# Kernel tuning notes

Hardware: AMD Instinct MI355X
Metric: run time of the kernel (lower is better)

## Reference

```python
import jax, jax.numpy as jnp
import numpy as np


def _dilate(x, ker):
    """Grayscale (max-plus) dilation, TF tf.nn.dilation2d semantics, SAME pad, stride 1.

    x:   [B,H,W,C] or [B,H,W,C,F]
    ker: [kh,kw,C,F]
    out: [B,H,W,C,F] = max_{dy,dx} x_pad[b, h+dy, w+dx, c(,f)] + ker[dy,dx,c,f]
    """
    kh, kw = ker.shape[0], ker.shape[1]
    pt, pl = (kh - 1) // 2, (kw - 1) // 2
    pb, pr = kh - 1 - pt, kw - 1 - pl
    if x.ndim == 4:
        x = x[..., None]  # broadcast over filter axis
    B, H, W = x.shape[0], x.shape[1], x.shape[2]
    xp = jnp.pad(x, ((0, 0), (pt, pb), (pl, pr), (0, 0), (0, 0)),
                 constant_values=-jnp.inf)
    out = None
    for dy in range(kh):
        for dx in range(kw):
            v = xp[:, dy:dy + H, dx:dx + W] + ker[dy, dx]  # [B,H,W,C,F]
            out = v if out is None else jnp.maximum(out, v)
    return out


def _erode(x, ker):
    # TF identity: erosion2d(v, f) = -dilation2d(-v, spatially-flipped f)
    return -_dilate(-x, ker[::-1, ::-1])


def _opening_p4(x, kernel):
    # x: [B,4,H,W,C], kernel: [kh,kw,3,C,F]
    kero = jnp.stack([jnp.rot90(kernel[:, :, 2], 3, axes=(0, 1)),
                      kernel[:, :, 1],
                      jnp.rot90(kernel[:, :, 0], 1, axes=(0, 1))], axis=2)
    y = jnp.concatenate([x[:, -1:], x, x[:, :1]], axis=1)  # wrap group axis -> [B,6,H,W,C]
    ero = []
    for j in range(4):
        kr = jnp.rot90(kero, j, axes=(0, 1))  # [kh,kw,3,C,F]
        d = jnp.stack([_erode(y[:, j + k], kr[:, :, k]) for k in range(3)], axis=-1)
        ero.append(jnp.min(d, axis=-1))  # min over SE depth -> [B,H,W,C,F]
    ero = jnp.stack(ero, axis=1)  # [B,4,H,W,C,F]
    ep = jnp.concatenate([ero[:, -1:], ero, ero[:, :1]], axis=1)  # [B,6,H,W,C,F]
    outs = []
    for j in range(4):
        kr = jnp.rot90(kernel, j, axes=(0, 1))
        d = jnp.stack([_dilate(ep[:, j + k], kr[:, :, k]) for k in range(3)], axis=-1)
        outs.append(jnp.max(d, axis=-1))  # max over SE depth -> [B,H,W,C,F]
    open_res = jnp.stack(outs, axis=1)  # [B,4,H,W,C,F]
    return jnp.sum(open_res, axis=-2)   # sum over input channels -> [B,4,H,W,F]


def setup_inputs() -> dict:
    key = jax.random.key(0)
    k1, k2 = jax.random.split(key)
    x = jax.random.normal(k1, (4, 4, 64, 64, 8), dtype=jnp.float32)
    kernel = jax.random.normal(k2, (3, 3, 3, 8, 16), dtype=jnp.float32) * 0.1
    return {"x": x, "kernel": kernel}


def reference(x, kernel):
    return _opening_p4(x, kernel)
```

## Files before the change

### kernel.cpp

```cpp
#include <hip/hip_runtime.h>


#define HH 64
#define WW 64
#define NEG_INF (-__builtin_inff())
#define POS_INF (__builtin_inff())

#define ROT_G(G, A, B, I, J) do { switch (G) { \
    case 0:  I = (A);     J = (B);     break; \
    case 1:  I = (B);     J = 2 - (A); break; \
    case 2:  I = 2 - (A); J = 2 - (B); break; \
    default: I = 2 - (B); J = (A);     break; } } while (0)

typedef _Float16 hv4 __attribute__((ext_vector_type(4)));

__device__ __forceinline__ hv4 f4_to_hv4(float4 v) {
    hv4 r;
    r.x = (_Float16)v.x; r.y = (_Float16)v.y;
    r.z = (_Float16)v.z; r.w = (_Float16)v.w;
    return r;
}

__device__ __forceinline__ hv4 bcast16(float v) {
    _Float16 p = (_Float16)v;
    return (hv4){p, p, p, p};
}

__global__ __launch_bounds__(256) void erode_t(const float* __restrict__ x,
                                               const float* __restrict__ ker,
                                               hv4* __restrict__ ero) {
    __shared__ __align__(16) float xs[9 * 8 * 68];

    const int tid = threadIdx.x;
    const int h = blockIdx.x & 63;
    const int g = (blockIdx.x >> 6) & 3;
    const int b = blockIdx.x >> 8;

    const float4* x4 = (const float4*)x;
    const float4* ker4 = (const float4*)ker;

    for (int t = tid; t < 1188; t += 256) {
        int q01 = t & 1;
        int u = t >> 1;
        int wp = u % 66;
        int v = u / 66;
        int r = v % 3;
        int p = v / 3;
        int g2 = (g + p + 3) & 3;
        int h2 = h - 1 + r;
        int w2 = wp - 1;
        float4 vv;
        if ((unsigned)h2 < HH && (unsigned)w2 < WW)
            vv = x4[(((b * 4 + g2) * HH + h2) * WW + w2) * 2 + q01];
        else
            vv = make_float4(POS_INF, POS_INF, POS_INF, POS_INF);
        int rowb = (p * 3 + r) * 8 + q01 * 4;
        xs[(rowb + 0) * 68 + wp] = vv.x;
        xs[(rowb + 1) * 68 + wp] = vv.y;
        xs[(rowb + 2) * 68 + wp] = vv.z;
        xs[(rowb + 3) * 68 + wp] = vv.w;
    }
    __syncthreads();

    const int q = tid & 3;
    const int c = (tid >> 2) & 7;
    const int slot = tid >> 5;
    const float4* xs4 = (const float4*)xs;

    const _Float16 pinf16 = (_Float16)POS_INF;
    hv4 acc[8];
#pragma unroll
    for (int i = 0; i < 8; ++i)
        acc[i] = (hv4){pinf16, pinf16, pinf16, pinf16};

#pragma unroll
    for (int k2 = 0; k2 < 3; ++k2) {
        hv4 ke9[9];
#pragma unroll
        for (int t9 = 0; t9 < 9; ++t9) {
            int dy = t9 / 3, dx = t9 % 3;
            int a0 = 2 - dy, b0 = 2 - dx;
            int i, jj;
            ROT_G(g, a0, b0, i, jj);
            int ka, kb, kc;
            if (k2 == 0)      { ka = 2 - jj; kb = i;      kc = 2; }
            else if (k2 == 1) { ka = i;      kb = jj;     kc = 1; }
            else              { ka = jj;     kb = 2 - i;  kc = 0; }
            ke9[t9] = f4_to_hv4(ker4[((ka * 3 + kb) * 3 + kc) * 32 + c * 4 + q]);
        }
#pragma unroll
        for (int dy = 0; dy < 3; ++dy) {
            const int base4 = ((k2 * 3 + dy) * 8 + c) * 17 + slot * 2;
            float4 xa = xs4[base4];
            float4 xb = xs4[base4 + 1];
            float4 xc = xs4[base4 + 2];
            float xw[12] = {xa.x, xa.y, xa.z, xa.w,
                            xb.x, xb.y, xb.z, xb.w,
                            xc.x, xc.y, xc.z, xc.w};
            hv4 xv[12];
#pragma unroll
            for (int i = 0; i < 12; ++i)
                xv[i] = bcast16(xw[i]);
#pragma unroll
            for (int dx = 0; dx < 3; ++dx) {
                hv4 kv = ke9[dy * 3 + dx];
#pragma unroll
                for (int i = 0; i < 8; ++i)
                    acc[i] = __builtin_elementwise_min(acc[i], xv[i + dx] - kv);
            }
        }
    }

    const int row = (b * 4 + g) * HH + h;
    const size_t obase = ((size_t)row * 66 + slot * 8 + 1) * 32 + c * 4 + q;
#pragma unroll
    for (int i = 0; i < 8; ++i)
        ero[obase + (size_t)i * 32] = acc[i];

    const hv4 ninf = {(_Float16)NEG_INF, (_Float16)NEG_INF,
                      (_Float16)NEG_INF, (_Float16)NEG_INF};
    if (tid < 32)
        ero[(size_t)row * 66 * 32 + tid] = ninf;
    else if (tid < 64)
        ero[((size_t)row * 66 + 65) * 32 + (tid - 32)] = ninf;
}

__global__ __launch_bounds__(256) void dilate_t(const hv4* __restrict__ ero,
                                                const float* __restrict__ ker,
                                                float* __restrict__ out) {
    const int tid = threadIdx.x;
    const int q = tid & 3;
    const int c = (tid >> 2) & 7;
    const int slot = tid >> 5;
    const int ws = blockIdx.x & 7;
    const int hs = (blockIdx.x >> 3) & 7;
    const int j = (blockIdx.x >> 6) & 3;
    const int b = blockIdx.x >> 8;
    const int w = ws * 8 + slot;

    const float4* ker4 = (const float4*)ker;

    const hv4 ninf = {(_Float16)NEG_INF, (_Float16)NEG_INF,
                      (_Float16)NEG_INF, (_Float16)NEG_INF};
    hv4 acc[8];
#pragma unroll
    for (int r = 0; r < 8; ++r)
        acc[r] = ninf;

#pragma unroll
    for (int k = 0; k < 3; ++k) {
        const int gsrc = (j + k + 3) & 3;
        hv4 kd9[9];
#pragma unroll
        for (int t9 = 0; t9 < 9; ++t9) {
            int dy = t9 / 3, dx = t9 % 3;
            int i, jj;
            ROT_G(j, dy, dx, i, jj);
            kd9[t9] = f4_to_hv4(ker4[((i * 3 + jj) * 3 + k) * 32 + c * 4 + q]);
        }
        const size_t pb = ((size_t)(b * 4 + gsrc) * HH * 66 + w) * 32 + c * 4 + q;
#pragma unroll
        for (int ei = 0; ei < 10; ++ei) {
            const int er = hs * 8 - 1 + ei;
            if ((unsigned)er >= HH) continue;
            const size_t rb = pb + (size_t)er * 66 * 32;
            hv4 e0 = ero[rb];
            hv4 e1 = ero[rb + 32];
            hv4 e2 = ero[rb + 64];
#pragma unroll
            for (int dy = 0; dy < 3; ++dy) {
                const int rr = ei - dy;
                if ((unsigned)rr >= 8) continue;
                acc[rr] = __builtin_elementwise_max(acc[rr], e0 + kd9[dy * 3 + 0]);
                acc[rr] = __builtin_elementwise_max(acc[rr], e1 + kd9[dy * 3 + 1]);
                acc[rr] = __builtin_elementwise_max(acc[rr], e2 + kd9[dy * 3 + 2]);
            }
        }
    }

    float4* out4 = (float4*)out;
    const int bjbase = (b * 4 + j) * HH + hs * 8;
#pragma unroll
    for (int r = 0; r < 8; ++r) {
        float4 s = make_float4((float)acc[r].x, (float)acc[r].y,
                               (float)acc[r].z, (float)acc[r].w);
#pragma unroll
        for (int off = 4; off <= 16; off <<= 1) {
            s.x += __shfl_xor(s.x, off, 64);
            s.y += __shfl_xor(s.y, off, 64);
            s.z += __shfl_xor(s.z, off, 64);
            s.w += __shfl_xor(s.w, off, 64);
        }
        if (c == 0)
            out4[((size_t)(bjbase + r) * WW + w) * 4 + q] = s;
    }
}

__global__ __launch_bounds__(256, 3) void opening_fused_fb(
    const float* __restrict__ x, const float* __restrict__ ker, float* __restrict__ out)
{
    __shared__ __align__(16) float xs[8 * 4 * 144];
    __shared__ float4 es4[4 * 4 * 100];
    __shared__ float4 ke4[27 * 4 * 4];
    __shared__ float4 kd4[9 * 4 * 4];

    const int tid = threadIdx.x;
    const int tileX = blockIdx.x & 7;
    const int tileY = (blockIdx.x >> 3) & 7;
    const int j = (blockIdx.x >> 6) & 3;
    const int b = blockIdx.x >> 8;
    const float4* ker4 = (const float4*)ker;
    const float4* x4 = (const float4*)x;

    for (int t = tid; t < 1152; t += 256) {
        int q01 = t & 1;
        int cell = t >> 1;
        int g = cell / 144;
        int rem = cell - g * 144;
        int r = rem / 12;
        int s = rem - r * 12;
        int h = tileY * 8 - 2 + r;
        int w = tileX * 8 - 2 + s;
        float4 v;
        if ((unsigned)h < HH && (unsigned)w < WW)
            v = x4[(((b * 4 + g) * HH + h) * WW + w) * 2 + q01];
        else
            v = make_float4(POS_INF, POS_INF, POS_INF, POS_INF);
        int c0 = q01 * 4;
        xs[((c0 + 0) * 4 + g) * 144 + rem] = v.x;
        xs[((c0 + 1) * 4 + g) * 144 + rem] = v.y;
        xs[((c0 + 2) * 4 + g) * 144 + rem] = v.z;
        xs[((c0 + 3) * 4 + g) * 144 + rem] = v.w;
    }
    __syncthreads();

    const int q_o = tid & 3;
    const int ox = (tid >> 2) & 7;
    const int oy = tid >> 5;

    float4 acc[8];
#pragma unroll
    for (int c = 0; c < 8; ++c)
        acc[c] = make_float4(NEG_INF, NEG_INF, NEG_INF, NEG_INF);

    for (int k = 0; k < 3; ++k) {
        const int gsrc = (j + k + 3) & 3;
#pragma unroll
        for (int cg = 0; cg < 2; ++cg) {
            for (int t = tid; t < 576; t += 256) {
                if (t < 432) {
                    int q = t & 3;
                    int c4 = (t >> 2) & 3;
                    int tap = t >> 4;
                    int k2 = tap % 3;
                    int dxdy = tap / 3;
                    int dx = dxdy % 3;
                    int dy = dxdy / 3;
                    int a0 = 2 - dy, b0 = 2 - dx;
                    int i, jj;
                    ROT_G(gsrc, a0, b0, i, jj);
                    int ka, kb, kc;
                    if (k2 == 0)      { ka = 2 - jj; kb = i;      kc = 2; }
                    else if (k2 == 1) { ka = i;      kb = jj;     kc = 1; }
                    else              { ka = jj;     kb = 2 - i;  kc = 0; }
                    int c = cg * 4 + c4;
                    ke4[t] = ker4[((ka * 3 + kb) * 3 + kc) * 32 + c * 4 + q];
                } else {
                    int u = t - 432;
                    int q = u & 3;
                    int c4 = (u >> 2) & 3;
                    int dydx = u >> 4;
                    int dx = dydx % 3;
                    int dy = dydx / 3;
                    int i, jj;
                    ROT_G(j, dy, dx, i, jj);
                    int c = cg * 4 + c4;
                    kd4[u] = ker4[((i * 3 + jj) * 3 + k) * 32 + c * 4 + q];
                }
            }
            __syncthreads();

            for (int it = 0; it < 2; ++it) {
                int id = tid + (it << 8);
                int c4 = id >> 7;
                int p = id & 127;
                if (p >= 100) continue;
                int ey = (p * 205) >> 11;
                int ex = p - ey * 10;
                int h_es = tileY * 8 - 1 + ey;
                int w_es = tileX * 8 - 1 + ex;
                float4 b0, b1, b2, b3;
                if ((unsigned)h_es < HH && (unsigned)w_es < WW) {
                    b0 = b1 = b2 = b3 = make_float4(POS_INF, POS_INF, POS_INF, POS_INF);
                    int c = cg * 4 + c4;
#pragma unroll
                    for (int k2 = 0; k2 < 3; ++k2) {
                        int g2 = (gsrc + k2 + 3) & 3;
                        int base = (c * 4 + g2) * 144 + ey * 12 + ex;
#pragma unroll
                        for (int dy = 0; dy < 3; ++dy)
#pragma unroll
                            for (int dx = 0; dx < 3; ++dx) {
                                float v = xs[base + dy * 12 + dx];
                                const float4* kk = &ke4[(((dy * 3 + dx) * 3 + k2) * 4 + c4) * 4];
                                float4 kv;
                                kv = kk[0];
                                b0.x = fminf(b0.x, v - kv.x); b0.y = fminf(b0.y, v - kv.y);
                                b0.z = fminf(b0.z, v - kv.z); b0.w = fminf(b0.w, v - kv.w);
                                kv = kk[1];
                                b1.x = fminf(b1.x, v - kv.x); b1.y = fminf(b1.y, v - kv.y);
                                b1.z = fminf(b1.z, v - kv.z); b1.w = fminf(b1.w, v - kv.w);
                                kv = kk[2];
                                b2.x = fminf(b2.x, v - kv.x); b2.y = fminf(b2.y, v - kv.y);
                                b2.z = fminf(b2.z, v - kv.z); b2.w = fminf(b2.w, v - kv.w);
                                kv = kk[3];
                                b3.x = fminf(b3.x, v - kv.x); b3.y = fminf(b3.y, v - kv.y);
                                b3.z = fminf(b3.z, v - kv.z); b3.w = fminf(b3.w, v - kv.w);
                            }
                    }
                } else {
                    b0 = b1 = b2 = b3 = make_float4(NEG_INF, NEG_INF, NEG_INF, NEG_INF);
                }
                int eb = (c4 * 4) * 100 + p;
                es4[eb] = b0; es4[eb + 100] = b1; es4[eb + 200] = b2; es4[eb + 300] = b3;
            }
            __syncthreads();

#pragma unroll
            for (int c4 = 0; c4 < 4; ++c4) {
                float4 a = acc[cg * 4 + c4];
#pragma unroll
                for (int dy = 0; dy < 3; ++dy)
#pragma unroll
                    for (int dx = 0; dx < 3; ++dx) {
                        int pos = (oy + dy) * 10 + (ox + dx);
                        float4 e = es4[(c4 * 4 + q_o) * 100 + pos];
                        float4 kv = kd4[(dy * 3 + dx) * 16 + c4 * 4 + q_o];
                        a.x = fmaxf(a.x, e.x + kv.x);
                        a.y = fmaxf(a.y, e.y + kv.y);
                        a.z = fmaxf(a.z, e.z + kv.z);
                        a.w = fmaxf(a.w, e.w + kv.w);
                    }
                acc[cg * 4 + c4] = a;
            }
            __syncthreads();
        }
    }

    float4 s = acc[0];
#pragma unroll
    for (int c = 1; c < 8; ++c) {
        s.x += acc[c].x; s.y += acc[c].y; s.z += acc[c].z; s.w += acc[c].w;
    }
    const int h = tileY * 8 + oy;
    const int w = tileX * 8 + ox;
    ((float4*)out)[(((b * 4 + j) * HH + h) * WW + w) * 4 + q_o] = s;
}

extern "C" void kernel_launch(void* const* d_in, const int* in_sizes, int n_in,
                              void* d_out, int out_size, void* d_ws, size_t ws_size,
                              hipStream_t stream) {
    const float* x = (const float*)d_in[0];
    const float* ker = (const float*)d_in[1];
    float* out = (float*)d_out;

    const size_t ero_f16_bytes = (size_t)16 * HH * 66 * 32 * 8;

    if (ws_size >= ero_f16_bytes) {
        hv4* ero = (hv4*)d_ws;
        erode_t<<<1024, 256, 0, stream>>>(x, ker, ero);
        dilate_t<<<1024, 256, 0, stream>>>(ero, ker, out);
    } else {
        opening_fused_fb<<<1024, 256, 0, stream>>>(x, ker, out);
    }
}
```

Baseline: 91.92 us.

## Compute all four output rotations per dilate block to reuse eroded rows

The dilate kernel now loops over each source group once and scatters its contribution into all three output rotations that depend on it, holding accumulators for all four rotations at four rows each. Each eroded row is loaded once per source group instead of being reloaded for every output rotation, which cuts global/L2 traffic. The price is more registers (16 accumulators plus 27 kernel vectors), a smaller grid of 512 blocks, and a larger relative halo with 4-row tiles.

```diff
diff --git a/kernel.cpp b/kernel.cpp
--- a/kernel.cpp
+++ b/kernel.cpp
@@ -125,75 +125,87 @@
         ero[((size_t)row * 66 + 65) * 32 + (tid - 32)] = ninf;
 }
 
-__global__ __launch_bounds__(256) void dilate_t(const hv4* __restrict__ ero,
-                                                const float* __restrict__ ker,
-                                                float* __restrict__ out) {
+__global__ __launch_bounds__(256) void dilate_j4(const hv4* __restrict__ ero,
+                                                 const float* __restrict__ ker,
+                                                 float* __restrict__ out) {
     const int tid = threadIdx.x;
     const int q = tid & 3;
     const int c = (tid >> 2) & 7;
     const int slot = tid >> 5;
-    const int ws = blockIdx.x & 7;
-    const int hs = (blockIdx.x >> 3) & 7;
-    const int j = (blockIdx.x >> 6) & 3;
-    const int b = blockIdx.x >> 8;
+    const int idx = blockIdx.x;
+    const int ws = idx & 7;
+    const int hs = (idx >> 3) & 15;
+    const int b = idx >> 7;
     const int w = ws * 8 + slot;
 
     const float4* ker4 = (const float4*)ker;
 
     const hv4 ninf = {(_Float16)NEG_INF, (_Float16)NEG_INF,
                       (_Float16)NEG_INF, (_Float16)NEG_INF};
-    hv4 acc[8];
-#pragma unroll
-    for (int r = 0; r < 8; ++r)
-        acc[r] = ninf;
-
-#pragma unroll
-    for (int k = 0; k < 3; ++k) {
-        const int gsrc = (j + k + 3) & 3;
-        hv4 kd9[9];
-#pragma unroll
-        for (int t9 = 0; t9 < 9; ++t9) {
-            int dy = t9 / 3, dx = t9 % 3;
-            int i, jj;
-            ROT_G(j, dy, dx, i, jj);
-            kd9[t9] = f4_to_hv4(ker4[((i * 3 + jj) * 3 + k) * 32 + c * 4 + q]);
+    hv4 acc[4][4];
+#pragma unroll
+    for (int jp = 0; jp < 4; ++jp)
+#pragma unroll
+        for (int rr = 0; rr < 4; ++rr)
+            acc[jp][rr] = ninf;
+
+#pragma unroll
+    for (int gsrc = 0; gsrc < 4; ++gsrc) {
+        hv4 kd[3][9];
+#pragma unroll
+        for (int k = 0; k < 3; ++k) {
+            const int jp = (gsrc + 1 - k + 4) & 3;
+#pragma unroll
+            for (int t9 = 0; t9 < 9; ++t9) {
+                int dy = t9 / 3, dx = t9 % 3;
+                int i, jj;
+                ROT_G(jp, dy, dx, i, jj);
+                kd[k][t9] = f4_to_hv4(ker4[((i * 3 + jj) * 3 + k) * 32 + c * 4 + q]);
+            }
         }
         const size_t pb = ((size_t)(b * 4 + gsrc) * HH * 66 + w) * 32 + c * 4 + q;
 #pragma unroll
-        for (int ei = 0; ei < 10; ++ei) {
-            const int er = hs * 8 - 1 + ei;
+        for (int ei = 0; ei < 6; ++ei) {
+            const int er = hs * 4 - 1 + ei;
             if ((unsigned)er >= HH) continue;
             const size_t rb = pb + (size_t)er * 66 * 32;
             hv4 e0 = ero[rb];
             hv4 e1 = ero[rb + 32];
             hv4 e2 = ero[rb + 64];
 #pragma unroll
-            for (int dy = 0; dy < 3; ++dy) {
-                const int rr = ei - dy;
-                if ((unsigned)rr >= 8) continue;
-                acc[rr] = __builtin_elementwise_max(acc[rr], e0 + kd9[dy * 3 + 0]);
-                acc[rr] = __builtin_elementwise_max(acc[rr], e1 + kd9[dy * 3 + 1]);
-                acc[rr] = __builtin_elementwise_max(acc[rr], e2 + kd9[dy * 3 + 2]);
+            for (int k = 0; k < 3; ++k) {
+                const int jp = (gsrc + 1 - k + 4) & 3;
+#pragma unroll
+                for (int dy = 0; dy < 3; ++dy) {
+                    const int rr = ei - dy;
+                    if ((unsigned)rr >= 4) continue;
+                    acc[jp][rr] = __builtin_elementwise_max(acc[jp][rr], e0 + kd[k][dy * 3 + 0]);
+                    acc[jp][rr] = __builtin_elementwise_max(acc[jp][rr], e1 + kd[k][dy * 3 + 1]);
+                    acc[jp][rr] = __builtin_elementwise_max(acc[jp][rr], e2 + kd[k][dy * 3 + 2]);
+                }
             }
         }
     }
 
     float4* out4 = (float4*)out;
-    const int bjbase = (b * 4 + j) * HH + hs * 8;
-#pragma unroll
-    for (int r = 0; r < 8; ++r) {
-        float4 s = make_float4((float)acc[r].x, (float)acc[r].y,
-                               (float)acc[r].z, (float)acc[r].w);
-#pragma unroll
-        for (int off = 4; off <= 16; off <<= 1) {
-            s.x += __shfl_xor(s.x, off, 64);
-            s.y += __shfl_xor(s.y, off, 64);
-            s.z += __shfl_xor(s.z, off, 64);
-            s.w += __shfl_xor(s.w, off, 64);
-        }
-        if (c == 0)
-            out4[((size_t)(bjbase + r) * WW + w) * 4 + q] = s;
-    }
+#pragma unroll
+    for (int jp = 0; jp < 4; ++jp)
+#pragma unroll
+        for (int rr = 0; rr < 4; ++rr) {
+            hv4 a = acc[jp][rr];
+            float4 s = make_float4((float)a.x, (float)a.y, (float)a.z, (float)a.w);
+#pragma unroll
+            for (int off = 4; off <= 16; off <<= 1) {
+                s.x += __shfl_xor(s.x, off, 64);
+                s.y += __shfl_xor(s.y, off, 64);
+                s.z += __shfl_xor(s.z, off, 64);
+                s.w += __shfl_xor(s.w, off, 64);
+            }
+            if (c == 0) {
+                const int row = (b * 4 + jp) * HH + hs * 4 + rr;
+                out4[((size_t)row * WW + w) * 4 + q] = s;
+            }
+        }
 }
 
 __global__ __launch_bounds__(256, 3) void opening_fused_fb(
@@ -369,7 +381,7 @@
     if (ws_size >= ero_f16_bytes) {
         hv4* ero = (hv4*)d_ws;
         erode_t<<<1024, 256, 0, stream>>>(x, ker, ero);
-        dilate_t<<<1024, 256, 0, stream>>>(ero, ker, out);
+        dilate_j4<<<512, 256, 0, stream>>>(ero, ker, out);
     } else {
         opening_fused_fb<<<1024, 256, 0, stream>>>(x, ker, out);
     }
```

Result: slower. 106.2 us (+15.5%).
